# Kernel optimization log

Hardware: AMD Instinct MI355X
Metric: run time of the kernel (lower is better)

## Reference

```python
import jax, jax.numpy as jnp
import numpy as np

EPS = 1e-8

def unit_normalize(x):
    # x / max(||x||_2, eps) along last dim (matches F.normalize semantics)
    n = jnp.sqrt(jnp.sum(x * x, axis=-1, keepdims=True))
    return x / jnp.maximum(n, EPS)

def setup_inputs() -> dict:
    key = jax.random.key(0)
    k1, k2, k3, k4 = jax.random.split(key, 4)
    BS, N, B, r, D = 8, 4096, 8, 64, 256
    q = jax.random.normal(k1, (BS, N, B, D), dtype=jnp.float32)
    pm_K = unit_normalize(jax.random.normal(k2, (BS, B, r, D), dtype=jnp.float32))
    pm_V = jax.random.normal(k3, (BS, B, r, D), dtype=jnp.float32)
    pm_a = jax.random.uniform(k4, (BS, B, r), dtype=jnp.float32)
    return {"q": q, "pm_K": pm_K, "pm_V": pm_V, "pm_a": pm_a}

def reference(q, pm_K, pm_V, pm_a):
    # Holographic read: q [BS,N,B,D], pm_K/pm_V [BS,B,r,D], pm_a [BS,B,r]
    q_norm = unit_normalize(q)
    # scores = normalize(q) @ pm_K^T  -> [BS,N,B,r]
    scores = jnp.einsum('snbd,sbrd->snbr', q_norm, pm_K)
    # slot-strength scaling
    weighted = scores * pm_a[:, None, :, :]
    # modulation = weighted @ pm_V -> [BS,N,B,D]
    modulation = jnp.einsum('snbr,sbrd->snbd', weighted, pm_V)
    return q * modulation
```

## Files before the change

kernel.cpp:

```cpp
#include <hip/hip_runtime.h>

#define BS 8
#define NN 4096
#define NB 8
#define NR 64
#define ND 256
#define TN 128
#define QPAD 264
#define SPAD 72

typedef __attribute__((ext_vector_type(8))) short bf16x8;
typedef __attribute__((ext_vector_type(4))) float f32x4;

__device__ __forceinline__ unsigned short f2bf(float f) {
    unsigned int u = __builtin_bit_cast(unsigned int, f);
    u += 0x7fffu + ((u >> 16) & 1u);
    return (unsigned short)(u >> 16);
}
__device__ __forceinline__ float bf2f(unsigned short h) {
    unsigned int u = ((unsigned int)h) << 16;
    return __builtin_bit_cast(float, u);
}

__global__ __launch_bounds__(512, 2)
void holo_read_kernel(const float* __restrict__ q,
                      const float* __restrict__ pmK,
                      const float* __restrict__ pmV,
                      const float* __restrict__ pma,
                      float* __restrict__ out)
{
    __shared__ __attribute__((aligned(16))) unsigned short qbf[TN][QPAD];
    __shared__ __attribute__((aligned(16))) unsigned short Kb[NR][QPAD];
    __shared__ __attribute__((aligned(16))) unsigned short Vt[ND][SPAD];
    __shared__ __attribute__((aligned(16))) unsigned short Ssm[TN][SPAD];
    __shared__ float invn[TN];
    __shared__ float a_sh[NR];

    const int tid  = threadIdx.x;
    const int lane = tid & 63;
    const int w    = tid >> 6;
    const int ln15 = lane & 15;
    const int quad = lane >> 4;

    const int sbi   = blockIdx.x & 63;
    const int chunk = blockIdx.x >> 6;
    const int s     = sbi >> 3;
    const int b     = sbi & 7;

    if (tid < NR) a_sh[tid] = pma[sbi * NR + tid];
    const size_t kvbase = (size_t)sbi * NR * ND;
    for (int rr = w; rr < NR; rr += 8) {
        const float4 kv = *(const float4*)&pmK[kvbase + (size_t)rr * ND + lane * 4];
        ushort4 uk;
        uk.x = f2bf(kv.x); uk.y = f2bf(kv.y); uk.z = f2bf(kv.z); uk.w = f2bf(kv.w);
        *(ushort4*)&Kb[rr][lane * 4] = uk;
        const float4 vv = *(const float4*)&pmV[kvbase + (size_t)rr * ND + lane * 4];
        Vt[lane * 4 + 0][rr] = f2bf(vv.x);
        Vt[lane * 4 + 1][rr] = f2bf(vv.y);
        Vt[lane * 4 + 2][rr] = f2bf(vv.z);
        Vt[lane * 4 + 3][rr] = f2bf(vv.w);
    }
    __syncthreads();

    for (int t = 0; t < 8; ++t) {
        const int n0 = (chunk * 8 + t) * TN;

        for (int base = 0; base < 16; base += 4) {
            float4 bufv[4];
            #pragma unroll
            for (int j = 0; j < 4; ++j) {
                const int row = (base + j) * 8 + w;
                const size_t gb = ((size_t)(s * NN + n0 + row) * NB + b) * ND;
                bufv[j] = *(const float4*)&q[gb + lane * 4];
            }
            #pragma unroll
            for (int j = 0; j < 4; ++j) {
                const int row = (base + j) * 8 + w;
                const float4 qv = bufv[j];
                float ss = qv.x * qv.x + qv.y * qv.y + qv.z * qv.z + qv.w * qv.w;
                #pragma unroll
                for (int m = 1; m < 64; m <<= 1) ss += __shfl_xor(ss, m, 64);
                if (lane == 0) invn[row] = 1.0f / fmaxf(sqrtf(ss), 1e-8f);
                ushort4 uq;
                uq.x = f2bf(qv.x); uq.y = f2bf(qv.y); uq.z = f2bf(qv.z); uq.w = f2bf(qv.w);
                *(ushort4*)&qbf[row][lane * 4] = uq;
            }
        }
        __syncthreads();

        {
            f32x4 accS[4];
            #pragma unroll
            for (int rt = 0; rt < 4; ++rt) accS[rt] = (f32x4){0.f, 0.f, 0.f, 0.f};
            #pragma unroll
            for (int kk = 0; kk < 8; ++kk) {
                const bf16x8 afr = *(const bf16x8*)&qbf[16 * w + ln15][kk * 32 + quad * 8];
                #pragma unroll
                for (int rt = 0; rt < 4; ++rt) {
                    const bf16x8 bfr = *(const bf16x8*)&Kb[rt * 16 + ln15][kk * 32 + quad * 8];
                    accS[rt] = __builtin_amdgcn_mfma_f32_16x16x32_bf16(afr, bfr, accS[rt], 0, 0, 0);
                }
            }
            float inr[4];
            #pragma unroll
            for (int reg = 0; reg < 4; ++reg) inr[reg] = invn[16 * w + quad * 4 + reg];
            #pragma unroll
            for (int rt = 0; rt < 4; ++rt) {
                const float ar = a_sh[rt * 16 + ln15];
                #pragma unroll
                for (int reg = 0; reg < 4; ++reg) {
                    Ssm[16 * w + quad * 4 + reg][rt * 16 + ln15] = f2bf(accS[rt][reg] * ar * inr[reg]);
                }
            }
        }
        __syncthreads();

        {
            f32x4 accO[16];
            #pragma unroll
            for (int dt = 0; dt < 16; ++dt) accO[dt] = (f32x4){0.f, 0.f, 0.f, 0.f};
            #pragma unroll
            for (int kt = 0; kt < 2; ++kt) {
                const bf16x8 aw = *(const bf16x8*)&Ssm[16 * w + ln15][kt * 32 + quad * 8];
                #pragma unroll
                for (int dt = 0; dt < 16; ++dt) {
                    const bf16x8 bv = *(const bf16x8*)&Vt[dt * 16 + ln15][kt * 32 + quad * 8];
                    accO[dt] = __builtin_amdgcn_mfma_f32_16x16x32_bf16(aw, bv, accO[dt], 0, 0, 0);
                }
            }
            #pragma unroll
            for (int reg = 0; reg < 4; ++reg) {
                const int n = 16 * w + quad * 4 + reg;
                const size_t gb = ((size_t)(s * NN + n0 + n) * NB + b) * ND;
                #pragma unroll
                for (int dt = 0; dt < 16; ++dt) {
                    const int d = dt * 16 + ln15;
                    out[gb + d] = bf2f(qbf[n][d]) * accO[dt][reg];
                }
            }
        }
        __syncthreads();
    }
}

extern "C" void kernel_launch(void* const* d_in, const int* in_sizes, int n_in,
                              void* d_out, int out_size, void* d_ws, size_t ws_size,
                              hipStream_t stream) {
    const float* q   = (const float*)d_in[0];
    const float* pmK = (const float*)d_in[1];
    const float* pmV = (const float*)d_in[2];
    const float* pma = (const float*)d_in[3];
    float* out = (float*)d_out;
    (void)in_sizes; (void)n_in; (void)out_size; (void)d_ws; (void)ws_size;
    hipLaunchKernelGGL(holo_read_kernel, dim3(256), dim3(512), 0, stream,
                       q, pmK, pmV, pma, out);
}
```

Before: 450.0 us.

## Register-prefetch q tiles per wave and remove block-wide barriers from main loop

Each wave now owns its 16 rows end to end. It loads its q fragments straight into registers and prefetches the next tile's q while computing the current one. It reads the A operand from registers instead of LDS and applies the row norm at output time, so the invn shared array and all per-iteration __syncthreads go away. The second MFMA swaps operands, so each lane stores contiguous float4 outputs instead of scattered scalar stores. This adds register pressure (16 float4 prefetch, 8 bf16x8 fragments and 16 accumulators), which could reduce occupancy at launch bounds of 512 threads with 2 blocks.

```diff
diff --git a/kernel.cpp b/kernel.cpp
--- a/kernel.cpp
+++ b/kernel.cpp
@@ -33,7 +33,6 @@
     __shared__ __attribute__((aligned(16))) unsigned short Kb[NR][QPAD];
     __shared__ __attribute__((aligned(16))) unsigned short Vt[ND][SPAD];
     __shared__ __attribute__((aligned(16))) unsigned short Ssm[TN][SPAD];
-    __shared__ float invn[TN];
     __shared__ float a_sh[NR];
 
     const int tid  = threadIdx.x;
@@ -46,6 +45,21 @@
     const int chunk = blockIdx.x >> 6;
     const int s     = sbi >> 3;
     const int b     = sbi & 7;
+
+    const int myrow = w * 16 + ln15;
+    const size_t row_stride = (size_t)NB * ND;
+    const float* qbase = q   + ((size_t)(s * NN + chunk * 1024 + myrow) * NB + b) * ND + quad * 8;
+    float*       obase = out + ((size_t)(s * NN + chunk * 1024 + myrow) * NB + b) * ND;
+
+    float4 pf[16];
+    {
+        const float* p = qbase;
+        #pragma unroll
+        for (int kk = 0; kk < 8; ++kk) {
+            pf[2 * kk]     = *(const float4*)(p + kk * 32);
+            pf[2 * kk + 1] = *(const float4*)(p + kk * 32 + 4);
+        }
+    }
 
     if (tid < NR) a_sh[tid] = pma[sbi * NR + tid];
     const size_t kvbase = (size_t)sbi * NR * ND;
@@ -62,84 +76,83 @@
     }
     __syncthreads();
 
-    for (int t = 0; t < 8; ++t) {
-        const int n0 = (chunk * 8 + t) * TN;
+    float ar[4];
+    #pragma unroll
+    for (int rt = 0; rt < 4; ++rt) ar[rt] = a_sh[rt * 16 + ln15];
 
-        for (int base = 0; base < 16; base += 4) {
-            float4 bufv[4];
+    for (int it = 0; it < 8; ++it) {
+        float ss = 0.f;
+        bf16x8 qfrag[8];
+        #pragma unroll
+        for (int kk = 0; kk < 8; ++kk) {
+            const float4 v0 = pf[2 * kk], v1 = pf[2 * kk + 1];
+            ss += v0.x * v0.x + v0.y * v0.y + v0.z * v0.z + v0.w * v0.w
+                + v1.x * v1.x + v1.y * v1.y + v1.z * v1.z + v1.w * v1.w;
+            bf16x8 f;
+            f[0] = (short)f2bf(v0.x); f[1] = (short)f2bf(v0.y);
+            f[2] = (short)f2bf(v0.z); f[3] = (short)f2bf(v0.w);
+            f[4] = (short)f2bf(v1.x); f[5] = (short)f2bf(v1.y);
+            f[6] = (short)f2bf(v1.z); f[7] = (short)f2bf(v1.w);
+            qfrag[kk] = f;
+            *(bf16x8*)&qbf[myrow][kk * 32 + quad * 8] = f;
+        }
+
+        if (it < 7) {
+            const float* p = qbase + (size_t)(it + 1) * 128 * row_stride;
             #pragma unroll
-            for (int j = 0; j < 4; ++j) {
-                const int row = (base + j) * 8 + w;
-                const size_t gb = ((size_t)(s * NN + n0 + row) * NB + b) * ND;
-                bufv[j] = *(const float4*)&q[gb + lane * 4];
-            }
-            #pragma unroll
-            for (int j = 0; j < 4; ++j) {
-                const int row = (base + j) * 8 + w;
-                const float4 qv = bufv[j];
-                float ss = qv.x * qv.x + qv.y * qv.y + qv.z * qv.z + qv.w * qv.w;
-                #pragma unroll
-                for (int m = 1; m < 64; m <<= 1) ss += __shfl_xor(ss, m, 64);
-                if (lane == 0) invn[row] = 1.0f / fmaxf(sqrtf(ss), 1e-8f);
-                ushort4 uq;
-                uq.x = f2bf(qv.x); uq.y = f2bf(qv.y); uq.z = f2bf(qv.z); uq.w = f2bf(qv.w);
-                *(ushort4*)&qbf[row][lane * 4] = uq;
+            for (int kk = 0; kk < 8; ++kk) {
+                pf[2 * kk]     = *(const float4*)(p + kk * 32);
+                pf[2 * kk + 1] = *(const float4*)(p + kk * 32 + 4);
             }
         }
-        __syncthreads();
 
-        {
-            f32x4 accS[4];
-            #pragma unroll
-            for (int rt = 0; rt < 4; ++rt) accS[rt] = (f32x4){0.f, 0.f, 0.f, 0.f};
-            #pragma unroll
-            for (int kk = 0; kk < 8; ++kk) {
-                const bf16x8 afr = *(const bf16x8*)&qbf[16 * w + ln15][kk * 32 + quad * 8];
-                #pragma unroll
-                for (int rt = 0; rt < 4; ++rt) {
-                    const bf16x8 bfr = *(const bf16x8*)&Kb[rt * 16 + ln15][kk * 32 + quad * 8];
-                    accS[rt] = __builtin_amdgcn_mfma_f32_16x16x32_bf16(afr, bfr, accS[rt], 0, 0, 0);
-                }
-            }
-            float inr[4];
-            #pragma unroll
-            for (int reg = 0; reg < 4; ++reg) inr[reg] = invn[16 * w + quad * 4 + reg];
+        ss += __shfl_xor(ss, 16, 64);
+        ss += __shfl_xor(ss, 32, 64);
+        const float inv = 1.0f / fmaxf(sqrtf(ss), 1e-8f);
+
+        f32x4 accS[4];
+        #pragma unroll
+        for (int rt = 0; rt < 4; ++rt) accS[rt] = (f32x4){0.f, 0.f, 0.f, 0.f};
+        #pragma unroll
+        for (int kk = 0; kk < 8; ++kk) {
             #pragma unroll
             for (int rt = 0; rt < 4; ++rt) {
-                const float ar = a_sh[rt * 16 + ln15];
-                #pragma unroll
-                for (int reg = 0; reg < 4; ++reg) {
-                    Ssm[16 * w + quad * 4 + reg][rt * 16 + ln15] = f2bf(accS[rt][reg] * ar * inr[reg]);
-                }
+                const bf16x8 bfr = *(const bf16x8*)&Kb[rt * 16 + ln15][kk * 32 + quad * 8];
+                accS[rt] = __builtin_amdgcn_mfma_f32_16x16x32_bf16(qfrag[kk], bfr, accS[rt], 0, 0, 0);
             }
         }
-        __syncthreads();
-
-        {
-            f32x4 accO[16];
-            #pragma unroll
-            for (int dt = 0; dt < 16; ++dt) accO[dt] = (f32x4){0.f, 0.f, 0.f, 0.f};
-            #pragma unroll
-            for (int kt = 0; kt < 2; ++kt) {
-                const bf16x8 aw = *(const bf16x8*)&Ssm[16 * w + ln15][kt * 32 + quad * 8];
-                #pragma unroll
-                for (int dt = 0; dt < 16; ++dt) {
-                    const bf16x8 bv = *(const bf16x8*)&Vt[dt * 16 + ln15][kt * 32 + quad * 8];
-                    accO[dt] = __builtin_amdgcn_mfma_f32_16x16x32_bf16(aw, bv, accO[dt], 0, 0, 0);
-                }
-            }
+        #pragma unroll
+        for (int rt = 0; rt < 4; ++rt) {
             #pragma unroll
             for (int reg = 0; reg < 4; ++reg) {
-                const int n = 16 * w + quad * 4 + reg;
-                const size_t gb = ((size_t)(s * NN + n0 + n) * NB + b) * ND;
-                #pragma unroll
-                for (int dt = 0; dt < 16; ++dt) {
-                    const int d = dt * 16 + ln15;
-                    out[gb + d] = bf2f(qbf[n][d]) * accO[dt][reg];
-                }
+                Ssm[w * 16 + quad * 4 + reg][rt * 16 + ln15] = f2bf(accS[rt][reg] * ar[rt]);
             }
         }
-        __syncthreads();
+
+        f32x4 accO[16];
+        #pragma unroll
+        for (int dt = 0; dt < 16; ++dt) accO[dt] = (f32x4){0.f, 0.f, 0.f, 0.f};
+        #pragma unroll
+        for (int kt = 0; kt < 2; ++kt) {
+            const bf16x8 aw = *(const bf16x8*)&Ssm[myrow][kt * 32 + quad * 8];
+            #pragma unroll
+            for (int dt = 0; dt < 16; ++dt) {
+                const bf16x8 bv = *(const bf16x8*)&Vt[dt * 16 + ln15][kt * 32 + quad * 8];
+                accO[dt] = __builtin_amdgcn_mfma_f32_16x16x32_bf16(bv, aw, accO[dt], 0, 0, 0);
+            }
+        }
+
+        float* op = obase + (size_t)it * 128 * row_stride;
+        #pragma unroll
+        for (int dt = 0; dt < 16; ++dt) {
+            const ushort4 qb = *(const ushort4*)&qbf[myrow][dt * 16 + quad * 4];
+            float4 o;
+            o.x = bf2f(qb.x) * (inv * accO[dt][0]);
+            o.y = bf2f(qb.y) * (inv * accO[dt][1]);
+            o.z = bf2f(qb.z) * (inv * accO[dt][2]);
+            o.w = bf2f(qb.w) * (inv * accO[dt][3]);
+            *(float4*)(op + dt * 16 + quad * 4) = o;
+        }
     }
 }
 
```

Result: slower. 551.6 us (+22.6%).
